# Kernel optimization log

Measured on AMD Instinct MI355X. Metric: run time of the kernel, lower is better.

Reference implementation:

```python
import jax, jax.numpy as jnp
import numpy as np

N, C, H, W = 1, 1, 4096, 4096

def setup_inputs() -> dict:
    key = jax.random.key(0)
    x = jax.random.normal(key, (N, C, H, W), dtype=jnp.float32)
    return {"x": x}

def reference(x):
    # torch.median returns the lower of the two middle values for even counts:
    # take the k-th smallest with k = (n-1)//2.
    n = x.size
    median = jnp.sort(x.reshape(-1))[(n - 1) // 2]
    # threshold everything below the median to zero
    thresholded = jnp.where(x < median, jnp.float32(0.0), x)
    # 7x7 max pool, stride 1, padding 3 (torch pads with -inf for max pool)
    pooled = jax.lax.reduce_window(
        thresholded,
        -jnp.inf,
        jax.lax.max,
        window_dimensions=(1, 1, 7, 7),
        window_strides=(1, 1, 1, 1),
        padding=[(0, 0), (0, 0), (3, 3), (3, 3)],
    )
    # In the original, gather(flatten(thresholded), max_indices) == pooled,
    # so binarize where the thresholded value equals its local window max.
    binarized = jnp.where(thresholded == pooled, jnp.float32(1.0), jnp.float32(0.0))
    return binarized * x
```

## Files before the change

### kernel.cpp

```cpp
#include <hip/hip_runtime.h>
#include <math.h>

#define IMG_H 4096
#define IMG_W 4096
#define TS 64
#define HALO 3
#define TW 70
#define THS 71
#define HMS 65
#define NBINS 4096
#define CBLK 1024
#define CAPA 1024
#define CAND_MAX (1u<<22)
#define WLO (-0.001953125f)
#define WHI ( 0.001953125f)
#define RSLOT 32
#define MCAP 1024
#define NSUB 2048

struct SelState {
    unsigned bin;
    unsigned k_rem;
    float    median;
    unsigned flag;
};

__device__ __forceinline__ unsigned f2u(float f) {
    unsigned b = __float_as_uint(f);
    unsigned mask = (unsigned)(-(int)(b >> 31)) | 0x80000000u;
    return b ^ mask;
}
__device__ __forceinline__ float u2f(unsigned u) {
    unsigned mask = (u >> 31) ? 0x80000000u : 0xFFFFFFFFu;
    return __uint_as_float(u ^ mask);
}

__device__ __forceinline__ int val_bin(float v) {
    float t = (v + 4.0f) * 512.0f;
    int b = (int)t;
    b = b < 0 ? 0 : b;
    b = b > (NBINS - 1) ? (NBINS - 1) : b;
    return b;
}

__device__ __forceinline__ int sub_bin(float v) {
    float t = (v - WLO) * (float)(NSUB * 256);
    int b = (int)t;
    b = b < 0 ? 0 : b;
    b = b > (NSUB - 1) ? (NSUB - 1) : b;
    return b;
}

__global__ __launch_bounds__(512) void count_compact(
    const float4* __restrict__ x4, int n4,
    unsigned* __restrict__ belowArr,
    unsigned* __restrict__ candA, unsigned* __restrict__ cntA)
{
    __shared__ unsigned buf[CAPA];
    __shared__ unsigned wred[8];
    __shared__ unsigned lcnt, gbase;
    const int t = threadIdx.x;
    if (t == 0) lcnt = 0;
    __syncthreads();

    unsigned below = 0;
    int idx = blockIdx.x * 512 + t;
    int stride = gridDim.x * 512;
    for (int i = idx; i < n4; i += stride) {
        float4 v = x4[i];
        float vs[4] = {v.x, v.y, v.z, v.w};
        #pragma unroll
        for (int j = 0; j < 4; j++) {
            float vv = vs[j];
            below += (vv < WLO) ? 1u : 0u;
            if (vv >= WLO && vv < WHI) {
                unsigned p = atomicAdd(&lcnt, 1u);
                unsigned key = f2u(vv);
                if (p < CAPA) buf[p] = key;
                else { unsigned q = atomicAdd(cntA, 1u); if (q < CAND_MAX) candA[q] = key; }
            }
        }
    }
    #pragma unroll
    for (int off = 32; off >= 1; off >>= 1) below += __shfl_down(below, off, 64);
    if ((t & 63) == 0) wred[t >> 6] = below;
    __syncthreads();
    if (t == 0) {
        unsigned tot = 0;
        #pragma unroll
        for (int w = 0; w < 8; w++) tot += wred[w];
        belowArr[blockIdx.x] = tot;
        gbase = atomicAdd(cntA, (lcnt > CAPA) ? CAPA : lcnt);
    }
    __syncthreads();
    unsigned m = lcnt; if (m > CAPA) m = CAPA;
    for (unsigned i = t; i < m; i += 512) {
        unsigned q = gbase + i;
        if (q < CAND_MAX) candA[q] = buf[i];
    }
}

__global__ __launch_bounds__(1024) void finalize_kernel(
    const unsigned* __restrict__ belowArr,
    const unsigned* __restrict__ candA, const unsigned* __restrict__ cntA,
    unsigned K, SelState* __restrict__ st)
{
    __shared__ unsigned hist[NSUB];
    __shared__ unsigned mem[MCAP];
    __shared__ unsigned wsum[16];
    __shared__ unsigned s_below, s_sb, s_kr2, mcnt;
    const int t = threadIdx.x;
    const unsigned lane = t & 63, wid = t >> 6;

    unsigned b = (t < CBLK) ? belowArr[t] : 0u;
    #pragma unroll
    for (int off = 32; off >= 1; off >>= 1) b += __shfl_down(b, off, 64);
    if (lane == 0) wsum[wid] = b;
    if (t == 0) mcnt = 0;
    __syncthreads();
    if (t == 0) {
        unsigned tot = 0;
        #pragma unroll
        for (int w = 0; w < 16; w++) tot += wsum[w];
        s_below = tot;
    }
    __syncthreads();

    const unsigned below = s_below;
    const unsigned M = *cntA;
    const bool direct = (K >= below) && (K - below < M) && (M <= RSLOT * 1024u);
    if (!direct) return;

    const unsigned kRem = K - below;

    unsigned rc[RSLOT];
    #pragma unroll
    for (int j = 0; j < RSLOT; j++) {
        int i = j * 1024 + t;
        rc[j] = (i < (int)M) ? candA[i] : 0u;
    }
    for (int i = t; i < NSUB; i += 1024) hist[i] = 0;
    __syncthreads();

    #pragma unroll
    for (int j = 0; j < RSLOT; j++) {
        int i = j * 1024 + t;
        if (i < (int)M) atomicAdd(&hist[sub_bin(u2f(rc[j]))], 1u);
    }
    __syncthreads();

    unsigned d0 = hist[t * 2], d1 = hist[t * 2 + 1];
    unsigned loc2 = d0 + d1;
    unsigned s2 = loc2;
    #pragma unroll
    for (int off = 1; off < 64; off <<= 1) {
        unsigned u = __shfl_up(s2, off, 64);
        if (lane >= off) s2 += u;
    }
    if (lane == 63) wsum[wid] = s2;
    __syncthreads();
    unsigned base2 = 0;
    for (unsigned w = 0; w < wid; w++) base2 += wsum[w];
    unsigned excl2 = base2 + s2 - loc2;
    if (kRem >= excl2 && kRem < excl2 + loc2) {
        if (kRem < excl2 + d0) { s_sb = (unsigned)(t * 2);     s_kr2 = kRem - excl2; }
        else                   { s_sb = (unsigned)(t * 2 + 1); s_kr2 = kRem - excl2 - d0; }
    }
    __syncthreads();

    const int sb = (int)s_sb;
    #pragma unroll
    for (int j = 0; j < RSLOT; j++) {
        int i = j * 1024 + t;
        if (i < (int)M && sub_bin(u2f(rc[j])) == sb) {
            unsigned p = atomicAdd(&mcnt, 1u);
            if (p < MCAP) mem[p] = rc[j];
        }
    }
    __syncthreads();
    if (mcnt > MCAP) return;

    const unsigned m = mcnt;
    const unsigned kr2 = s_kr2;
    if ((unsigned)t < m) {
        unsigned ku = mem[t];
        unsigned c = 0, e = 0;
        for (unsigned j = 0; j < m; j++) {
            unsigned kj = mem[j];
            c += (kj < ku);
            e += (kj == ku);
        }
        if (c <= kr2 && kr2 < c + e) { st->median = u2f(ku); st->flag = 1; }
    }
}

__global__ __launch_bounds__(1024) void fb_exact(
    const float4* __restrict__ x4, int n4, unsigned K,
    unsigned* __restrict__ candB, SelState* __restrict__ st)
{
    if (st->flag) return;
    __shared__ unsigned lh[NBINS];
    __shared__ unsigned wsum[16];
    __shared__ unsigned s_bin, s_krem, s_m, s_pref, s_kr;
    const int t = threadIdx.x;
    const unsigned lane = t & 63, wid = t >> 6;

    for (int i = t; i < NBINS; i += 1024) lh[i] = 0;
    __syncthreads();
    for (int i = t; i < n4; i += 1024) {
        float4 v = x4[i];
        atomicAdd(&lh[val_bin(v.x)], 1u);
        atomicAdd(&lh[val_bin(v.y)], 1u);
        atomicAdd(&lh[val_bin(v.z)], 1u);
        atomicAdd(&lh[val_bin(v.w)], 1u);
    }
    __syncthreads();

    {
        unsigned cb[4];
        unsigned local = 0;
        #pragma unroll
        for (int j = 0; j < 4; j++) { cb[j] = lh[t * 4 + j]; local += cb[j]; }
        unsigned s = local;
        #pragma unroll
        for (int off = 1; off < 64; off <<= 1) {
            unsigned u = __shfl_up(s, off, 64);
            if (lane >= off) s += u;
        }
        if (lane == 63) wsum[wid] = s;
        __syncthreads();
        unsigned base = 0;
        for (unsigned w = 0; w < wid; w++) base += wsum[w];
        unsigned excl = base + s - local;
        if (K >= excl && K < excl + local) {
            unsigned cum = excl;
            #pragma unroll
            for (int j = 0; j < 4; j++) {
                if (K < cum + cb[j]) { s_bin = (unsigned)(t * 4 + j); s_krem = K - cum; break; }
                cum += cb[j];
            }
        }
        if (t == 0) s_m = 0;
        __syncthreads();
    }

    {
        const int b = (int)s_bin;
        for (int i = t; i < n4; i += 1024) {
            float4 v = x4[i];
            float vs[4] = {v.x, v.y, v.z, v.w};
            #pragma unroll
            for (int j = 0; j < 4; j++) {
                if (val_bin(vs[j]) == b) {
                    unsigned p = atomicAdd(&s_m, 1u);
                    candB[p] = f2u(vs[j]);
                }
            }
        }
        __syncthreads();
    }

    const int M = (int)s_m;
    if (t == 0) { s_pref = 0; s_kr = s_krem; }
    for (int p = 0; p < 3; p++) {
        const int shift = (p == 0) ? 21 : ((p == 1) ? 10 : 0);
        const int bits  = (p == 2) ? 10 : 11;
        const int nb    = 1 << bits;
        for (int i = t; i < nb; i += 1024) lh[i] = 0;
        __syncthreads();
        const unsigned pref = s_pref;
        for (int i = t; i < M; i += 1024) {
            unsigned u = candB[i];
            bool ok = (p == 0) || ((u >> ((p == 1) ? 21 : 10)) == pref);
            if (ok) atomicAdd(&lh[(u >> shift) & (unsigned)(nb - 1)], 1u);
        }
        __syncthreads();
        const int P = nb >> 10;
        unsigned c0 = lh[t * (P ? P : 1)];
        unsigned c1 = (P == 2) ? lh[t * 2 + 1] : 0u;
        unsigned valid = (P >= 1) || (t < nb);
        if (P == 0) { c0 = (t < nb) ? lh[t] : 0u; c1 = 0u; }
        unsigned local = valid ? (c0 + c1) : 0u;
        unsigned s = local;
        #pragma unroll
        for (int off = 1; off < 64; off <<= 1) {
            unsigned u = __shfl_up(s, off, 64);
            if (lane >= off) s += u;
        }
        if (lane == 63) wsum[wid] = s;
        __syncthreads();
        unsigned base = 0;
        for (unsigned w = 0; w < wid; w++) base += wsum[w];
        unsigned excl = base + s - local;
        unsigned kRem = s_kr;
        __syncthreads();
        if (kRem >= excl && kRem < excl + local) {
            if (P == 2) {
                if (kRem < excl + c0) { s_pref = (pref << bits) | (unsigned)(t * 2);     s_kr = kRem - excl; }
                else                  { s_pref = (pref << bits) | (unsigned)(t * 2 + 1); s_kr = kRem - excl - c0; }
            } else {
                s_pref = (pref << bits) | (unsigned)t;
                s_kr = kRem - excl;
            }
        }
        __syncthreads();
    }
    if (t == 0) st->median = u2f(s_pref);
}

__global__ __launch_bounds__(512) void nms_kernel(
    const float* __restrict__ x, float* __restrict__ out,
    const SelState* __restrict__ st)
{
    __shared__ float th[TW * THS];
    __shared__ float hm[TW * HMS];

    const float med = st->median;
    const float NEGINF = -__builtin_inff();
    const int bx = blockIdx.x, by = blockIdx.y;
    const int gy0 = by * TS - HALO;
    const int gcol0 = bx * TS - 4;

    for (int task = threadIdx.x; task < TW * 18; task += 512) {
        int r = task / 18, q = task - r * 18;
        int gy = gy0 + r;
        int gxb = gcol0 + q * 4;
        bool rowok = (gy >= 0 && gy < IMG_H);
        float vs[4];
        if (rowok && gxb >= 0 && gxb + 4 <= IMG_W) {
            float4 v = *(const float4*)&x[gy * IMG_W + gxb];
            vs[0] = v.x; vs[1] = v.y; vs[2] = v.z; vs[3] = v.w;
        } else if (rowok) {
            #pragma unroll
            for (int cmp = 0; cmp < 4; cmp++) {
                int gx = gxb + cmp;
                vs[cmp] = (gx >= 0 && gx < IMG_W) ? x[gy * IMG_W + gx] : NEGINF;
            }
        } else {
            vs[0] = vs[1] = vs[2] = vs[3] = NEGINF;
        }
        #pragma unroll
        for (int cmp = 0; cmp < 4; cmp++) {
            int c = q * 4 - 1 + cmp;
            if ((unsigned)c < (unsigned)TW) {
                float v = vs[cmp];
                v = (v == NEGINF) ? v : ((v < med) ? 0.0f : v);
                th[r * THS + c] = v;
            }
        }
    }
    __syncthreads();

    for (int task = threadIdx.x; task < TW * 8; task += 512) {
        int r = task % TW;
        int c0 = (task / TW) * 8;
        float w[7];
        #pragma unroll
        for (int i = 0; i < 14; i++) {
            w[i % 7] = th[r * THS + c0 + i];
            if (i >= 6) {
                float m = w[0];
                #pragma unroll
                for (int k = 1; k < 7; k++) m = fmaxf(m, w[k]);
                hm[r * HMS + c0 + i - 6] = m;
            }
        }
    }
    __syncthreads();

    {
        const int c = threadIdx.x & 63;
        const int rr0 = (threadIdx.x >> 6) * 8;
        float w[7];
        #pragma unroll
        for (int i = 0; i < 14; i++) {
            w[i % 7] = hm[(rr0 + i) * HMS + c];
            if (i >= 6) {
                int R = rr0 + i - 6;
                float m = w[0];
                #pragma unroll
                for (int k = 1; k < 7; k++) m = fmaxf(m, w[k]);
                float t = th[(R + HALO) * THS + (c + HALO)];
                int gy = by * TS + R;
                int gx = bx * TS + c;
                float o = 0.0f;
                if (t == m) {
                    o = (t != 0.0f) ? t : x[gy * IMG_W + gx];
                }
                out[gy * IMG_W + gx] = o;
            }
        }
    }
}

extern "C" void kernel_launch(void* const* d_in, const int* in_sizes, int n_in,
                              void* d_out, int out_size, void* d_ws, size_t ws_size,
                              hipStream_t stream)
{
    const float* x = (const float*)d_in[0];
    float* out = (float*)d_out;
    const int n = in_sizes[0];
    const unsigned K = (unsigned)((n - 1) / 2);

    char* ws = (char*)d_ws;
    unsigned* cntA     = (unsigned*)ws;
    SelState* st       = (SelState*)(ws + 16);
    unsigned* belowArr = (unsigned*)(ws + 256);
    unsigned* candA    = (unsigned*)(ws + ws_size / 2);

    hipMemsetAsync(d_ws, 0, 32, stream);

    const int n4 = n / 4;
    count_compact<<<CBLK, 512, 0, stream>>>((const float4*)x, n4, belowArr, candA, cntA);
    finalize_kernel<<<1, 1024, 0, stream>>>(belowArr, candA, cntA, K, st);
    fb_exact<<<1, 1024, 0, stream>>>((const float4*)x, n4, K, (unsigned*)d_out, st);

    dim3 fg(IMG_W / TS, IMG_H / TS);
    nms_kernel<<<fg, 512, 0, stream>>>(x, out, st);
}
```

Measured before the change: 148.4 us.

## Drop global atomics and memset, merge finalize/fallback kernels, fast-path interior tiles

Candidate compaction now writes into per-block fixed slots (CAPB per block) with per-block counts, which removes the global atomic counter and the workspace memset. The finalize and exact-fallback kernels are merged into one launch, and all loads in count_compact are issued up front when the size matches exactly. The NMS kernel gains a branch-free load path for interior tiles. In exchange, finalize walks each block's candidate list serially per thread, which may lengthen that single-block stage, and it falls back to the full histogram path if any block overflows its slot.

```diff
diff --git a/kernel.cpp b/kernel.cpp
--- a/kernel.cpp
+++ b/kernel.cpp
@@ -10,20 +10,13 @@
 #define HMS 65
 #define NBINS 4096
 #define CBLK 1024
-#define CAPA 1024
-#define CAND_MAX (1u<<22)
+#define CAPB 4096
 #define WLO (-0.001953125f)
 #define WHI ( 0.001953125f)
-#define RSLOT 32
 #define MCAP 1024
 #define NSUB 2048
 
-struct SelState {
-    unsigned bin;
-    unsigned k_rem;
-    float    median;
-    unsigned flag;
-};
+struct SelState { float median; };
 
 __device__ __forceinline__ unsigned f2u(float f) {
     unsigned b = __float_as_uint(f);
@@ -51,36 +44,56 @@
     return b;
 }
 
-__global__ __launch_bounds__(512) void count_compact(
+__global__ __launch_bounds__(512, 8) void count_compact(
     const float4* __restrict__ x4, int n4,
-    unsigned* __restrict__ belowArr,
-    unsigned* __restrict__ candA, unsigned* __restrict__ cntA)
+    unsigned* __restrict__ belowCnt,
+    unsigned* __restrict__ candCnt,
+    unsigned* __restrict__ candA)
 {
-    __shared__ unsigned buf[CAPA];
+    __shared__ unsigned buf[CAPB];
     __shared__ unsigned wred[8];
-    __shared__ unsigned lcnt, gbase;
+    __shared__ unsigned lcnt;
     const int t = threadIdx.x;
     if (t == 0) lcnt = 0;
     __syncthreads();
 
     unsigned below = 0;
-    int idx = blockIdx.x * 512 + t;
-    int stride = gridDim.x * 512;
-    for (int i = idx; i < n4; i += stride) {
-        float4 v = x4[i];
-        float vs[4] = {v.x, v.y, v.z, v.w};
-        #pragma unroll
-        for (int j = 0; j < 4; j++) {
-            float vv = vs[j];
-            below += (vv < WLO) ? 1u : 0u;
-            if (vv >= WLO && vv < WHI) {
-                unsigned p = atomicAdd(&lcnt, 1u);
-                unsigned key = f2u(vv);
-                if (p < CAPA) buf[p] = key;
-                else { unsigned q = atomicAdd(cntA, 1u); if (q < CAND_MAX) candA[q] = key; }
-            }
-        }
-    }
+    const int idx = blockIdx.x * 512 + t;
+    const int stride = CBLK * 512;
+
+    if (n4 == 8 * stride) {
+        float4 v[8];
+        #pragma unroll
+        for (int j = 0; j < 8; j++) v[j] = x4[idx + j * stride];
+        #pragma unroll
+        for (int j = 0; j < 8; j++) {
+            float vs[4] = {v[j].x, v[j].y, v[j].z, v[j].w};
+            #pragma unroll
+            for (int u = 0; u < 4; u++) {
+                float vv = vs[u];
+                below += (vv < WLO) ? 1u : 0u;
+                if (vv >= WLO && vv < WHI) {
+                    unsigned p = atomicAdd(&lcnt, 1u);
+                    if (p < CAPB) buf[p] = f2u(vv);
+                }
+            }
+        }
+    } else {
+        for (int i = idx; i < n4; i += stride) {
+            float4 v = x4[i];
+            float vs[4] = {v.x, v.y, v.z, v.w};
+            #pragma unroll
+            for (int u = 0; u < 4; u++) {
+                float vv = vs[u];
+                below += (vv < WLO) ? 1u : 0u;
+                if (vv >= WLO && vv < WHI) {
+                    unsigned p = atomicAdd(&lcnt, 1u);
+                    if (p < CAPB) buf[p] = f2u(vv);
+                }
+            }
+        }
+    }
+
     #pragma unroll
     for (int off = 32; off >= 1; off >>= 1) below += __shfl_down(below, off, 64);
     if ((t & 63) == 0) wred[t >> 6] = below;
@@ -89,122 +102,109 @@
         unsigned tot = 0;
         #pragma unroll
         for (int w = 0; w < 8; w++) tot += wred[w];
-        belowArr[blockIdx.x] = tot;
-        gbase = atomicAdd(cntA, (lcnt > CAPA) ? CAPA : lcnt);
-    }
-    __syncthreads();
-    unsigned m = lcnt; if (m > CAPA) m = CAPA;
-    for (unsigned i = t; i < m; i += 512) {
-        unsigned q = gbase + i;
-        if (q < CAND_MAX) candA[q] = buf[i];
-    }
-}
-
-__global__ __launch_bounds__(1024) void finalize_kernel(
-    const unsigned* __restrict__ belowArr,
-    const unsigned* __restrict__ candA, const unsigned* __restrict__ cntA,
-    unsigned K, SelState* __restrict__ st)
+        belowCnt[blockIdx.x] = tot;
+        candCnt[blockIdx.x] = lcnt;
+    }
+    unsigned m = lcnt; if (m > CAPB) m = CAPB;
+    const unsigned gbase = (unsigned)blockIdx.x * CAPB;
+    for (unsigned i = t; i < m; i += 512) candA[gbase + i] = buf[i];
+}
+
+__global__ __launch_bounds__(1024) void finalize_fb(
+    const float4* __restrict__ x4, int n4, unsigned K,
+    const unsigned* __restrict__ belowCnt,
+    const unsigned* __restrict__ candCnt,
+    const unsigned* __restrict__ candA,
+    unsigned* __restrict__ candB,
+    SelState* __restrict__ st)
 {
     __shared__ unsigned hist[NSUB];
     __shared__ unsigned mem[MCAP];
-    __shared__ unsigned wsum[16];
-    __shared__ unsigned s_below, s_sb, s_kr2, mcnt;
-    const int t = threadIdx.x;
-    const unsigned lane = t & 63, wid = t >> 6;
-
-    unsigned b = (t < CBLK) ? belowArr[t] : 0u;
-    #pragma unroll
-    for (int off = 32; off >= 1; off >>= 1) b += __shfl_down(b, off, 64);
-    if (lane == 0) wsum[wid] = b;
-    if (t == 0) mcnt = 0;
-    __syncthreads();
-    if (t == 0) {
-        unsigned tot = 0;
-        #pragma unroll
-        for (int w = 0; w < 16; w++) tot += wsum[w];
-        s_below = tot;
-    }
-    __syncthreads();
-
-    const unsigned below = s_below;
-    const unsigned M = *cntA;
-    const bool direct = (K >= below) && (K - below < M) && (M <= RSLOT * 1024u);
-    if (!direct) return;
-
-    const unsigned kRem = K - below;
-
-    unsigned rc[RSLOT];
-    #pragma unroll
-    for (int j = 0; j < RSLOT; j++) {
-        int i = j * 1024 + t;
-        rc[j] = (i < (int)M) ? candA[i] : 0u;
-    }
-    for (int i = t; i < NSUB; i += 1024) hist[i] = 0;
-    __syncthreads();
-
-    #pragma unroll
-    for (int j = 0; j < RSLOT; j++) {
-        int i = j * 1024 + t;
-        if (i < (int)M) atomicAdd(&hist[sub_bin(u2f(rc[j]))], 1u);
-    }
-    __syncthreads();
-
-    unsigned d0 = hist[t * 2], d1 = hist[t * 2 + 1];
-    unsigned loc2 = d0 + d1;
-    unsigned s2 = loc2;
-    #pragma unroll
-    for (int off = 1; off < 64; off <<= 1) {
-        unsigned u = __shfl_up(s2, off, 64);
-        if (lane >= off) s2 += u;
-    }
-    if (lane == 63) wsum[wid] = s2;
-    __syncthreads();
-    unsigned base2 = 0;
-    for (unsigned w = 0; w < wid; w++) base2 += wsum[w];
-    unsigned excl2 = base2 + s2 - loc2;
-    if (kRem >= excl2 && kRem < excl2 + loc2) {
-        if (kRem < excl2 + d0) { s_sb = (unsigned)(t * 2);     s_kr2 = kRem - excl2; }
-        else                   { s_sb = (unsigned)(t * 2 + 1); s_kr2 = kRem - excl2 - d0; }
-    }
-    __syncthreads();
-
-    const int sb = (int)s_sb;
-    #pragma unroll
-    for (int j = 0; j < RSLOT; j++) {
-        int i = j * 1024 + t;
-        if (i < (int)M && sub_bin(u2f(rc[j])) == sb) {
-            unsigned p = atomicAdd(&mcnt, 1u);
-            if (p < MCAP) mem[p] = rc[j];
-        }
-    }
-    __syncthreads();
-    if (mcnt > MCAP) return;
-
-    const unsigned m = mcnt;
-    const unsigned kr2 = s_kr2;
-    if ((unsigned)t < m) {
-        unsigned ku = mem[t];
-        unsigned c = 0, e = 0;
-        for (unsigned j = 0; j < m; j++) {
-            unsigned kj = mem[j];
-            c += (kj < ku);
-            e += (kj == ku);
-        }
-        if (c <= kr2 && kr2 < c + e) { st->median = u2f(ku); st->flag = 1; }
-    }
-}
-
-__global__ __launch_bounds__(1024) void fb_exact(
-    const float4* __restrict__ x4, int n4, unsigned K,
-    unsigned* __restrict__ candB, SelState* __restrict__ st)
-{
-    if (st->flag) return;
     __shared__ unsigned lh[NBINS];
-    __shared__ unsigned wsum[16];
+    __shared__ unsigned wsA[16], wsB[16], wsC[16];
+    __shared__ unsigned s_below, s_M, s_ovf, s_sb, s_kr2, mcnt;
     __shared__ unsigned s_bin, s_krem, s_m, s_pref, s_kr;
     const int t = threadIdx.x;
     const unsigned lane = t & 63, wid = t >> 6;
 
+    const unsigned cc = candCnt[t];
+    unsigned bsum = belowCnt[t];
+    unsigned csum = cc;
+    unsigned osum = (cc > CAPB) ? 1u : 0u;
+    #pragma unroll
+    for (int off = 32; off >= 1; off >>= 1) {
+        bsum += __shfl_down(bsum, off, 64);
+        csum += __shfl_down(csum, off, 64);
+        osum += __shfl_down(osum, off, 64);
+    }
+    if (lane == 0) { wsA[wid] = bsum; wsB[wid] = csum; wsC[wid] = osum; }
+    if (t == 0) mcnt = 0;
+    __syncthreads();
+    if (t == 0) {
+        unsigned b = 0, c = 0, o = 0;
+        #pragma unroll
+        for (int w = 0; w < 16; w++) { b += wsA[w]; c += wsB[w]; o += wsC[w]; }
+        s_below = b; s_M = c; s_ovf = o;
+    }
+    __syncthreads();
+
+    const unsigned below = s_below, M = s_M;
+    bool resolved = false;
+    if (s_ovf == 0u && K >= below && (K - below) < M) {
+        const unsigned kRem = K - below;
+        for (int i = t; i < NSUB; i += 1024) hist[i] = 0;
+        __syncthreads();
+
+        const unsigned base = (unsigned)t * CAPB;
+        for (unsigned i = 0; i < cc; i++)
+            atomicAdd(&hist[sub_bin(u2f(candA[base + i]))], 1u);
+        __syncthreads();
+
+        unsigned d0 = hist[t * 2], d1 = hist[t * 2 + 1];
+        unsigned loc2 = d0 + d1;
+        unsigned s2 = loc2;
+        #pragma unroll
+        for (int off = 1; off < 64; off <<= 1) {
+            unsigned u = __shfl_up(s2, off, 64);
+            if (lane >= off) s2 += u;
+        }
+        if (lane == 63) wsA[wid] = s2;
+        __syncthreads();
+        unsigned base2 = 0;
+        for (unsigned w = 0; w < wid; w++) base2 += wsA[w];
+        unsigned excl2 = base2 + s2 - loc2;
+        if (kRem >= excl2 && kRem < excl2 + loc2) {
+            if (kRem < excl2 + d0) { s_sb = (unsigned)(t * 2);     s_kr2 = kRem - excl2; }
+            else                   { s_sb = (unsigned)(t * 2 + 1); s_kr2 = kRem - excl2 - d0; }
+        }
+        __syncthreads();
+
+        const int sb = (int)s_sb;
+        for (unsigned i = 0; i < cc; i++) {
+            unsigned key = candA[base + i];
+            if (sub_bin(u2f(key)) == sb) {
+                unsigned p = atomicAdd(&mcnt, 1u);
+                if (p < MCAP) mem[p] = key;
+            }
+        }
+        __syncthreads();
+        if (mcnt <= MCAP) {
+            const unsigned m = mcnt, kr2 = s_kr2;
+            if ((unsigned)t < m) {
+                unsigned ku = mem[t], c = 0, e = 0;
+                for (unsigned j = 0; j < m; j++) {
+                    unsigned kj = mem[j];
+                    c += (kj < ku);
+                    e += (kj == ku);
+                }
+                if (c <= kr2 && kr2 < c + e) st->median = u2f(ku);
+            }
+            resolved = true;
+        }
+    }
+    if (resolved) return;
+
+    __syncthreads();
     for (int i = t; i < NBINS; i += 1024) lh[i] = 0;
     __syncthreads();
     for (int i = t; i < n4; i += 1024) {
@@ -227,10 +227,10 @@
             unsigned u = __shfl_up(s, off, 64);
             if (lane >= off) s += u;
         }
-        if (lane == 63) wsum[wid] = s;
+        if (lane == 63) wsA[wid] = s;
         __syncthreads();
         unsigned base = 0;
-        for (unsigned w = 0; w < wid; w++) base += wsum[w];
+        for (unsigned w = 0; w < wid; w++) base += wsA[w];
         unsigned excl = base + s - local;
         if (K >= excl && K < excl + local) {
             unsigned cum = excl;
@@ -260,7 +260,7 @@
         __syncthreads();
     }
 
-    const int M = (int)s_m;
+    const int M2 = (int)s_m;
     if (t == 0) { s_pref = 0; s_kr = s_krem; }
     for (int p = 0; p < 3; p++) {
         const int shift = (p == 0) ? 21 : ((p == 1) ? 10 : 0);
@@ -269,7 +269,7 @@
         for (int i = t; i < nb; i += 1024) lh[i] = 0;
         __syncthreads();
         const unsigned pref = s_pref;
-        for (int i = t; i < M; i += 1024) {
+        for (int i = t; i < M2; i += 1024) {
             unsigned u = candB[i];
             bool ok = (p == 0) || ((u >> ((p == 1) ? 21 : 10)) == pref);
             if (ok) atomicAdd(&lh[(u >> shift) & (unsigned)(nb - 1)], 1u);
@@ -278,29 +278,28 @@
         const int P = nb >> 10;
         unsigned c0 = lh[t * (P ? P : 1)];
         unsigned c1 = (P == 2) ? lh[t * 2 + 1] : 0u;
-        unsigned valid = (P >= 1) || (t < nb);
         if (P == 0) { c0 = (t < nb) ? lh[t] : 0u; c1 = 0u; }
-        unsigned local = valid ? (c0 + c1) : 0u;
+        unsigned local = c0 + c1;
         unsigned s = local;
         #pragma unroll
         for (int off = 1; off < 64; off <<= 1) {
             unsigned u = __shfl_up(s, off, 64);
             if (lane >= off) s += u;
         }
-        if (lane == 63) wsum[wid] = s;
+        if (lane == 63) wsA[wid] = s;
         __syncthreads();
         unsigned base = 0;
-        for (unsigned w = 0; w < wid; w++) base += wsum[w];
+        for (unsigned w = 0; w < wid; w++) base += wsA[w];
         unsigned excl = base + s - local;
-        unsigned kRem = s_kr;
-        __syncthreads();
-        if (kRem >= excl && kRem < excl + local) {
+        unsigned kRem2 = s_kr;
+        __syncthreads();
+        if (kRem2 >= excl && kRem2 < excl + local) {
             if (P == 2) {
-                if (kRem < excl + c0) { s_pref = (pref << bits) | (unsigned)(t * 2);     s_kr = kRem - excl; }
-                else                  { s_pref = (pref << bits) | (unsigned)(t * 2 + 1); s_kr = kRem - excl - c0; }
+                if (kRem2 < excl + c0) { s_pref = (pref << bits) | (unsigned)(t * 2);     s_kr = kRem2 - excl; }
+                else                   { s_pref = (pref << bits) | (unsigned)(t * 2 + 1); s_kr = kRem2 - excl - c0; }
             } else {
                 s_pref = (pref << bits) | (unsigned)t;
-                s_kr = kRem - excl;
+                s_kr = kRem2 - excl;
             }
         }
         __syncthreads();
@@ -321,31 +320,49 @@
     const int gy0 = by * TS - HALO;
     const int gcol0 = bx * TS - 4;
 
-    for (int task = threadIdx.x; task < TW * 18; task += 512) {
-        int r = task / 18, q = task - r * 18;
-        int gy = gy0 + r;
-        int gxb = gcol0 + q * 4;
-        bool rowok = (gy >= 0 && gy < IMG_H);
-        float vs[4];
-        if (rowok && gxb >= 0 && gxb + 4 <= IMG_W) {
-            float4 v = *(const float4*)&x[gy * IMG_W + gxb];
-            vs[0] = v.x; vs[1] = v.y; vs[2] = v.z; vs[3] = v.w;
-        } else if (rowok) {
+    if (bx >= 1 && bx <= (IMG_W / TS) - 2 && by >= 1 && by <= (IMG_H / TS) - 2) {
+        #pragma unroll
+        for (int k = 0; k < 3; k++) {
+            int task = threadIdx.x + k * 512;
+            if (task < TW * 18) {
+                int r = task / 18, q = task - r * 18;
+                const float4 v = *(const float4*)&x[(gy0 + r) * IMG_W + (gcol0 + q * 4)];
+                float vs[4] = {v.x, v.y, v.z, v.w};
+                #pragma unroll
+                for (int cmp = 0; cmp < 4; cmp++) {
+                    int c = q * 4 - 1 + cmp;
+                    if ((unsigned)c < (unsigned)TW)
+                        th[r * THS + c] = (vs[cmp] < med) ? 0.0f : vs[cmp];
+                }
+            }
+        }
+    } else {
+        for (int task = threadIdx.x; task < TW * 18; task += 512) {
+            int r = task / 18, q = task - r * 18;
+            int gy = gy0 + r;
+            int gxb = gcol0 + q * 4;
+            bool rowok = (gy >= 0 && gy < IMG_H);
+            float vs[4];
+            if (rowok && gxb >= 0 && gxb + 4 <= IMG_W) {
+                float4 v = *(const float4*)&x[gy * IMG_W + gxb];
+                vs[0] = v.x; vs[1] = v.y; vs[2] = v.z; vs[3] = v.w;
+            } else if (rowok) {
+                #pragma unroll
+                for (int cmp = 0; cmp < 4; cmp++) {
+                    int gx = gxb + cmp;
+                    vs[cmp] = (gx >= 0 && gx < IMG_W) ? x[gy * IMG_W + gx] : NEGINF;
+                }
+            } else {
+                vs[0] = vs[1] = vs[2] = vs[3] = NEGINF;
+            }
             #pragma unroll
             for (int cmp = 0; cmp < 4; cmp++) {
-                int gx = gxb + cmp;
-                vs[cmp] = (gx >= 0 && gx < IMG_W) ? x[gy * IMG_W + gx] : NEGINF;
-            }
-        } else {
-            vs[0] = vs[1] = vs[2] = vs[3] = NEGINF;
-        }
-        #pragma unroll
-        for (int cmp = 0; cmp < 4; cmp++) {
-            int c = q * 4 - 1 + cmp;
-            if ((unsigned)c < (unsigned)TW) {
-                float v = vs[cmp];
-                v = (v == NEGINF) ? v : ((v < med) ? 0.0f : v);
-                th[r * THS + c] = v;
+                int c = q * 4 - 1 + cmp;
+                if ((unsigned)c < (unsigned)TW) {
+                    float v = vs[cmp];
+                    v = (v == NEGINF) ? v : ((v < med) ? 0.0f : v);
+                    th[r * THS + c] = v;
+                }
             }
         }
     }
@@ -403,18 +420,17 @@
     const unsigned K = (unsigned)((n - 1) / 2);
 
     char* ws = (char*)d_ws;
-    unsigned* cntA     = (unsigned*)ws;
-    SelState* st       = (SelState*)(ws + 16);
-    unsigned* belowArr = (unsigned*)(ws + 256);
+    SelState* st       = (SelState*)ws;
+    unsigned* belowCnt = (unsigned*)(ws + 1024);
+    unsigned* candCnt  = (unsigned*)(ws + 1024 + 4096);
     unsigned* candA    = (unsigned*)(ws + ws_size / 2);
 
-    hipMemsetAsync(d_ws, 0, 32, stream);
-
     const int n4 = n / 4;
-    count_compact<<<CBLK, 512, 0, stream>>>((const float4*)x, n4, belowArr, candA, cntA);
-    finalize_kernel<<<1, 1024, 0, stream>>>(belowArr, candA, cntA, K, st);
-    fb_exact<<<1, 1024, 0, stream>>>((const float4*)x, n4, K, (unsigned*)d_out, st);
-
+    count_compact<<<CBLK, 512, 0, stream>>>((const float4*)x, n4,
+                                            belowCnt, candCnt, candA);
+    finalize_fb<<<1, 1024, 0, stream>>>((const float4*)x, n4, K,
+                                        belowCnt, candCnt, candA,
+                                        (unsigned*)d_out, st);
     dim3 fg(IMG_W / TS, IMG_H / TS);
     nms_kernel<<<fg, 512, 0, stream>>>(x, out, st);
 }
```

Result: slower. 152.5 us (+2.8%).
